# Optimization experiments

Hardware: AMD Instinct MI355X
Metric: run time of the kernel (lower is better)

Reference implementation:

```python
import jax, jax.numpy as jnp
import numpy as np

L = 10


def setup_inputs() -> dict:
    key = jax.random.key(0)
    ks = jax.random.split(key, L + 1)
    N = 1_000_000
    inp = {"points": jax.random.normal(ks[0], (N, 3), dtype=jnp.float32)}
    inp["cob_1"] = jax.random.normal(ks[1], (3, 3), dtype=jnp.float32)
    for l in range(2, L + 1):
        # [2l+1, 3*(2l-1)] change-of-basis matrix for angular order l
        inp[f"cob_{l}"] = jax.random.normal(ks[l], (2 * l + 1, 3 * (2 * l - 1)), dtype=jnp.float32)
    return inp


def _harmonic_forward(points, cobs):
    # points: [..., 3]; cobs: list of L matrices (cob_1 .. cob_L)
    shape = points.shape[:-1]
    f0 = jnp.ones(shape + (1,), dtype=points.dtype)
    # order-1 feature: [..., 3]
    f1 = jnp.einsum('...i,ji->...j', points, cobs[0])
    feats = [f0, f1]
    prev = f1
    for l in range(2, L + 1):
        cob = cobs[l - 1]  # [2l+1, 3*(2l-1)]
        # outer product of previous order feature with order-1 feature, flattened
        f = jnp.einsum('...i,...j->...ij', prev, f1).reshape(shape + (-1,))  # [..., 3*(2l-1)]
        f = jnp.einsum('...i,ji->...j', f, cob)  # [..., 2l+1]
        feats.append(f)
        prev = f
    return jnp.concatenate(feats, axis=-1)  # [..., (L+1)^2]


def reference(points, cob_1, cob_2, cob_3, cob_4, cob_5, cob_6, cob_7, cob_8, cob_9, cob_10):
    cobs = [cob_1, cob_2, cob_3, cob_4, cob_5, cob_6, cob_7, cob_8, cob_9, cob_10]
    return _harmonic_forward(points, cobs)
```

## Files before the change

### kernel.cpp

```cpp
#include <hip/hip_runtime.h>

#define BS 256
#define NFEAT 121
#define SMAX 37


__device__ __forceinline__ float dot3(const float* __restrict__ c, float x, float y, float z) {
    return fmaf(c[2], z, fmaf(c[1], y, c[0] * x));
}

template<int LL, bool UPDATE_PREV>
__device__ __forceinline__ void step_l(const float* __restrict__ cob,
                                       float* srow, int colofs,
                                       float f1x, float f1y, float f1z,
                                       float* prev) {
    constexpr int IN  = 2 * LL - 1;
    constexpr int OUT = 2 * LL + 1;
    #pragma unroll 1
    for (int j = 0; j < OUT; ++j) {
        const float* __restrict__ crow = cob + j * (3 * IN);
        float acc = 0.f;
        #pragma unroll
        for (int a = 0; a < IN; ++a)
            acc = fmaf(prev[a], dot3(crow + 3 * a, f1x, f1y, f1z), acc);
        srow[colofs + j] = acc;
    }
    if (UPDATE_PREV) {
        #pragma unroll
        for (int j = 0; j < OUT; ++j) prev[j] = srow[colofs + j];
    }
}

template<int W, int C0>
__device__ __forceinline__ void wave_drain(const float* slab, float* __restrict__ outw,
                                           int wrows, int lane) {
    if (lane < W) {
        const float* sp = slab + lane;
        float* __restrict__ gp = outw + C0 + lane;
        if (wrows == 64) {
            #pragma unroll 16
            for (int r = 0; r < 64; ++r)
                gp[r * NFEAT] = sp[r * SMAX];
        } else {
            #pragma unroll 4
            for (int r = 0; r < 64; ++r)
                if (r < wrows) gp[r * NFEAT] = sp[r * SMAX];
        }
    }
}

__global__ __launch_bounds__(BS) void harmonic_kernel(
    const float* __restrict__ points,
    const float* __restrict__ cob1,  const float* __restrict__ cob2,
    const float* __restrict__ cob3,  const float* __restrict__ cob4,
    const float* __restrict__ cob5,  const float* __restrict__ cob6,
    const float* __restrict__ cob7,  const float* __restrict__ cob8,
    const float* __restrict__ cob9,  const float* __restrict__ cob10,
    float* __restrict__ out, int N) {
    __shared__ float sbuf[(BS / 64) * 64 * SMAX];

    const int t    = threadIdx.x;
    const int lane = t & 63;
    const int w    = t >> 6;
    const long long wbase = (long long)blockIdx.x * BS + ((long long)w << 6);
    const long long p     = wbase + lane;
    const bool active = p < (long long)N;
    long long nv = (long long)N - wbase;
    const int wrows = nv >= 64 ? 64 : (nv > 0 ? (int)nv : 0);

    float px = 0.f, py = 0.f, pz = 0.f;
    if (active) {
        px = points[p * 3 + 0];
        py = points[p * 3 + 1];
        pz = points[p * 3 + 2];
    }

    const float f1x = dot3(cob1 + 0, px, py, pz);
    const float f1y = dot3(cob1 + 3, px, py, pz);
    const float f1z = dot3(cob1 + 6, px, py, pz);

    float prev[21];
    prev[0] = f1x; prev[1] = f1y; prev[2] = f1z;

    float* slab = sbuf + w * (64 * SMAX);
    float* srow = slab + lane * SMAX;
    float* __restrict__ outw = out + wbase * NFEAT;

    srow[0] = 1.f;
    srow[1] = f1x; srow[2] = f1y; srow[3] = f1z;
    step_l<2, true>(cob2, srow, 4,  f1x, f1y, f1z, prev);
    step_l<3, true>(cob3, srow, 9,  f1x, f1y, f1z, prev);
    step_l<4, true>(cob4, srow, 16, f1x, f1y, f1z, prev);
    step_l<5, true>(cob5, srow, 25, f1x, f1y, f1z, prev);
    wave_drain<36, 0>(slab, outw, wrows, lane);

    step_l<6, true>(cob6, srow, 0,  f1x, f1y, f1z, prev);
    step_l<7, true>(cob7, srow, 13, f1x, f1y, f1z, prev);
    wave_drain<28, 36>(slab, outw, wrows, lane);

    step_l<8, true>(cob8, srow, 0,  f1x, f1y, f1z, prev);
    step_l<9, true>(cob9, srow, 17, f1x, f1y, f1z, prev);
    wave_drain<36, 64>(slab, outw, wrows, lane);

    step_l<10, false>(cob10, srow, 0, f1x, f1y, f1z, prev);
    wave_drain<21, 100>(slab, outw, wrows, lane);
}

extern "C" void kernel_launch(void* const* d_in, const int* in_sizes, int n_in,
                              void* d_out, int out_size, void* d_ws, size_t ws_size,
                              hipStream_t stream) {
    const float* points = (const float*)d_in[0];
    const float* cob[10];
    for (int i = 0; i < 10; ++i) cob[i] = (const float*)d_in[1 + i];
    float* out = (float*)d_out;
    const int N = in_sizes[0] / 3;

    const int grid = (N + BS - 1) / BS;
    harmonic_kernel<<<grid, BS, 0, stream>>>(
        points,
        cob[0], cob[1], cob[2], cob[3], cob[4],
        cob[5], cob[6], cob[7], cob[8], cob[9],
        out, N);
}
```

Before: 801.5 us.

## Process two points per thread to amortize coefficient loads

```diff
diff --git a/kernel.cpp b/kernel.cpp
--- a/kernel.cpp
+++ b/kernel.cpp
@@ -2,32 +2,40 @@
 
 #define BS 256
 #define NFEAT 121
-#define SMAX 37
+#define SST 37
 
 
 __device__ __forceinline__ float dot3(const float* __restrict__ c, float x, float y, float z) {
     return fmaf(c[2], z, fmaf(c[1], y, c[0] * x));
 }
 
-template<int LL, bool UPDATE_PREV>
-__device__ __forceinline__ void step_l(const float* __restrict__ cob,
-                                       float* srow, int colofs,
-                                       float f1x, float f1y, float f1z,
-                                       float* prev) {
+template<int LL, bool UPD>
+__device__ __forceinline__ void step2(const float* __restrict__ cob,
+                                      float* srowA, float* srowB, int colofs,
+                                      float ax, float ay, float az,
+                                      float bx, float by, float bz,
+                                      float* prevA, float* prevB) {
     constexpr int IN  = 2 * LL - 1;
     constexpr int OUT = 2 * LL + 1;
-    #pragma unroll 1
+    #pragma unroll 2
     for (int j = 0; j < OUT; ++j) {
         const float* __restrict__ crow = cob + j * (3 * IN);
-        float acc = 0.f;
+        float accA = 0.f, accB = 0.f;
         #pragma unroll
-        for (int a = 0; a < IN; ++a)
-            acc = fmaf(prev[a], dot3(crow + 3 * a, f1x, f1y, f1z), acc);
-        srow[colofs + j] = acc;
+        for (int a = 0; a < IN; ++a) {
+            const float c0 = crow[3*a+0], c1 = crow[3*a+1], c2 = crow[3*a+2];
+            accA = fmaf(prevA[a], fmaf(c2, az, fmaf(c1, ay, c0 * ax)), accA);
+            accB = fmaf(prevB[a], fmaf(c2, bz, fmaf(c1, by, c0 * bx)), accB);
+        }
+        srowA[colofs + j] = accA;
+        srowB[colofs + j] = accB;
     }
-    if (UPDATE_PREV) {
+    if (UPD) {
         #pragma unroll
-        for (int j = 0; j < OUT; ++j) prev[j] = srow[colofs + j];
+        for (int j = 0; j < OUT; ++j) {
+            prevA[j] = srowA[colofs + j];
+            prevB[j] = srowB[colofs + j];
+        }
     }
 }
 
@@ -37,14 +45,14 @@
     if (lane < W) {
         const float* sp = slab + lane;
         float* __restrict__ gp = outw + C0 + lane;
-        if (wrows == 64) {
+        if (wrows == 128) {
             #pragma unroll 16
-            for (int r = 0; r < 64; ++r)
-                gp[r * NFEAT] = sp[r * SMAX];
+            for (int r = 0; r < 128; ++r)
+                gp[r * NFEAT] = sp[r * SST];
         } else {
             #pragma unroll 4
-            for (int r = 0; r < 64; ++r)
-                if (r < wrows) gp[r * NFEAT] = sp[r * SMAX];
+            for (int r = 0; r < 128; ++r)
+                if (r < wrows) gp[r * NFEAT] = sp[r * SST];
         }
     }
 }
@@ -57,52 +65,58 @@
     const float* __restrict__ cob7,  const float* __restrict__ cob8,
     const float* __restrict__ cob9,  const float* __restrict__ cob10,
     float* __restrict__ out, int N) {
-    __shared__ float sbuf[(BS / 64) * 64 * SMAX];
+    __shared__ float sbuf[(BS / 64) * 128 * SST];
 
     const int t    = threadIdx.x;
     const int lane = t & 63;
     const int w    = t >> 6;
-    const long long wbase = (long long)blockIdx.x * BS + ((long long)w << 6);
-    const long long p     = wbase + lane;
-    const bool active = p < (long long)N;
-    long long nv = (long long)N - wbase;
-    const int wrows = nv >= 64 ? 64 : (nv > 0 ? (int)nv : 0);
+    const long long wtile = (long long)blockIdx.x * ((BS / 64) * 128) + (long long)w * 128;
+    const long long pA = wtile + lane;
+    const long long pB = wtile + 64 + lane;
+    long long nv = (long long)N - wtile;
+    const int wrows = nv >= 128 ? 128 : (nv > 0 ? (int)nv : 0);
 
-    float px = 0.f, py = 0.f, pz = 0.f;
-    if (active) {
-        px = points[p * 3 + 0];
-        py = points[p * 3 + 1];
-        pz = points[p * 3 + 2];
+    float pax = 0.f, pay = 0.f, paz = 0.f, pbx = 0.f, pby = 0.f, pbz = 0.f;
+    if (pA < (long long)N) {
+        pax = points[pA * 3 + 0]; pay = points[pA * 3 + 1]; paz = points[pA * 3 + 2];
+    }
+    if (pB < (long long)N) {
+        pbx = points[pB * 3 + 0]; pby = points[pB * 3 + 1]; pbz = points[pB * 3 + 2];
     }
 
-    const float f1x = dot3(cob1 + 0, px, py, pz);
-    const float f1y = dot3(cob1 + 3, px, py, pz);
-    const float f1z = dot3(cob1 + 6, px, py, pz);
+    const float ax = dot3(cob1 + 0, pax, pay, paz);
+    const float ay = dot3(cob1 + 3, pax, pay, paz);
+    const float az = dot3(cob1 + 6, pax, pay, paz);
+    const float bx = dot3(cob1 + 0, pbx, pby, pbz);
+    const float by = dot3(cob1 + 3, pbx, pby, pbz);
+    const float bz = dot3(cob1 + 6, pbx, pby, pbz);
 
-    float prev[21];
-    prev[0] = f1x; prev[1] = f1y; prev[2] = f1z;
+    float prevA[21], prevB[21];
+    prevA[0] = ax; prevA[1] = ay; prevA[2] = az;
+    prevB[0] = bx; prevB[1] = by; prevB[2] = bz;
 
-    float* slab = sbuf + w * (64 * SMAX);
-    float* srow = slab + lane * SMAX;
-    float* __restrict__ outw = out + wbase * NFEAT;
+    float* slab  = sbuf + w * (128 * SST);
+    float* srowA = slab + lane * SST;
+    float* srowB = slab + (64 + lane) * SST;
+    float* __restrict__ outw = out + wtile * NFEAT;
 
-    srow[0] = 1.f;
-    srow[1] = f1x; srow[2] = f1y; srow[3] = f1z;
-    step_l<2, true>(cob2, srow, 4,  f1x, f1y, f1z, prev);
-    step_l<3, true>(cob3, srow, 9,  f1x, f1y, f1z, prev);
-    step_l<4, true>(cob4, srow, 16, f1x, f1y, f1z, prev);
-    step_l<5, true>(cob5, srow, 25, f1x, f1y, f1z, prev);
+    srowA[0] = 1.f; srowA[1] = ax; srowA[2] = ay; srowA[3] = az;
+    srowB[0] = 1.f; srowB[1] = bx; srowB[2] = by; srowB[3] = bz;
+    step2<2, true>(cob2, srowA, srowB, 4,  ax, ay, az, bx, by, bz, prevA, prevB);
+    step2<3, true>(cob3, srowA, srowB, 9,  ax, ay, az, bx, by, bz, prevA, prevB);
+    step2<4, true>(cob4, srowA, srowB, 16, ax, ay, az, bx, by, bz, prevA, prevB);
+    step2<5, true>(cob5, srowA, srowB, 25, ax, ay, az, bx, by, bz, prevA, prevB);
     wave_drain<36, 0>(slab, outw, wrows, lane);
 
-    step_l<6, true>(cob6, srow, 0,  f1x, f1y, f1z, prev);
-    step_l<7, true>(cob7, srow, 13, f1x, f1y, f1z, prev);
+    step2<6, true>(cob6, srowA, srowB, 0,  ax, ay, az, bx, by, bz, prevA, prevB);
+    step2<7, true>(cob7, srowA, srowB, 13, ax, ay, az, bx, by, bz, prevA, prevB);
     wave_drain<28, 36>(slab, outw, wrows, lane);
 
-    step_l<8, true>(cob8, srow, 0,  f1x, f1y, f1z, prev);
-    step_l<9, true>(cob9, srow, 17, f1x, f1y, f1z, prev);
+    step2<8, true>(cob8, srowA, srowB, 0,  ax, ay, az, bx, by, bz, prevA, prevB);
+    step2<9, true>(cob9, srowA, srowB, 17, ax, ay, az, bx, by, bz, prevA, prevB);
     wave_drain<36, 64>(slab, outw, wrows, lane);
 
-    step_l<10, false>(cob10, srow, 0, f1x, f1y, f1z, prev);
+    step2<10, false>(cob10, srowA, srowB, 0, ax, ay, az, bx, by, bz, prevA, prevB);
     wave_drain<21, 100>(slab, outw, wrows, lane);
 }
 
@@ -115,7 +129,8 @@
     float* out = (float*)d_out;
     const int N = in_sizes[0] / 3;
 
-    const int grid = (N + BS - 1) / BS;
+    const int ptsPerBlock = (BS / 64) * 128;
+    const int grid = (N + ptsPerBlock - 1) / ptsPerBlock;
     harmonic_kernel<<<grid, BS, 0, stream>>>(
         points,
         cob[0], cob[1], cob[2], cob[3], cob[4],
```

After: 825.3 us. 3.0% more time.
